# Kernel optimization log

Measured on AMD Instinct MI355X. Metric: run time of the kernel, lower is better.

The kernel has to match this reference:

```python
import jax, jax.numpy as jnp
import numpy as np

HIDDEN = 4096
NUM_BLOCKS = 8
BLOCK = HIDDEN // NUM_BLOCKS  # 512


def setup_inputs() -> dict:
    key = jax.random.key(0)
    k1, k2, k3, k4 = jax.random.split(key, 4)
    return {
        "weight": jax.random.normal(k1, (HIDDEN, HIDDEN), dtype=jnp.float32) * 0.02,
        "bias": jax.random.normal(k2, (HIDDEN,), dtype=jnp.float32) * 0.02,
        "x": jax.random.normal(k3, (4, 2048, HIDDEN), dtype=jnp.float32),
        "proj_R": jax.random.normal(k4, (NUM_BLOCKS, BLOCK, BLOCK), dtype=jnp.float32) * 0.02,
        "layer_idx": 0,
    }


def _cayley_batch(A):
    # Q = (I - S) @ inv(I + S + 1e-6*I), S = 0.5*(A - A^T), batched over blocks
    r = A.shape[-1]
    I = jnp.eye(r, dtype=A.dtype)
    S = 0.5 * (A - jnp.swapaxes(A, -2, -1))
    Minv = jnp.linalg.inv(I + S + 1e-6 * I)
    return jnp.einsum('bij,bjk->bik', I - S, Minv)


def reference(weight, bias, x, proj_R, layer_idx):
    Q = _cayley_batch(proj_R)                     # [nb, bs, bs], orthogonal blocks
    nb, bs, _ = Q.shape
    # block_diag(Q) @ weight == batched block-row matmul (off-diagonal blocks are zero)
    Wb = weight.reshape(nb, bs, weight.shape[1])  # [nb, bs, in]
    filt = jnp.einsum('bij,bjk->bik', Q, Wb).reshape(nb * bs, weight.shape[1])
    # F.linear(x, filt, bias)
    return jnp.einsum('bsi,oi->bso', x, filt) + bias
```

## Files before the change

kernel.cpp:

```cpp
#include <hip/hip_runtime.h>

typedef unsigned short u16;
typedef __attribute__((ext_vector_type(8))) short bf16x8;
typedef __attribute__((ext_vector_type(4))) float f32x4;
typedef __attribute__((ext_vector_type(8))) unsigned short u16x8;
typedef __attribute__((ext_vector_type(4))) unsigned short u16x4;

__device__ __forceinline__ u16 f2bf(float f){
  unsigned int u = __builtin_bit_cast(unsigned int, f);
  u += 0x7FFFu + ((u >> 16) & 1u);
  return (u16)(u >> 16);
}
__device__ __forceinline__ float bf2f(u16 h){
  unsigned int u = ((unsigned int)h) << 16;
  return __builtin_bit_cast(float, u);
}

__device__ __forceinline__ void load16(const u16* g, u16* s){
  __builtin_amdgcn_global_load_lds((const __attribute__((address_space(1))) unsigned int*)g,
                                   (__attribute__((address_space(3))) unsigned int*)s,
                                   16, 0, 0);
}

__global__ __launch_bounds__(256) void build_s(const float* __restrict__ R, u16* __restrict__ Sbf,
                                               u16* __restrict__ Dbf){
  int idx = blockIdx.x * 256 + threadIdx.x;
  int b = idx >> 18;
  int i = (idx >> 9) & 511;
  int j = idx & 511;
  float a  = R[idx];
  float at = R[(b << 18) + (j << 9) + i];
  float s = 0.5f * (a - at);
  Sbf[idx] = f2bf(s);
  Dbf[idx] = f2bf((i == j ? 2.000003f : 0.0f) - 2.000001f * s);
}

__global__ __launch_bounds__(256) void split_p(const float* __restrict__ P, u16* __restrict__ Phl,
                                               u16* __restrict__ X1, u16* __restrict__ X1d){
  int idx = blockIdx.x * 256 + threadIdx.x;
  int i = (idx >> 9) & 511;
  int j = idx & 511;
  float p = P[idx];
  u16 ph = f2bf(p);
  size_t rb = ((size_t)(idx >> 9)) << 10;
  Phl[rb + j]       = ph;
  Phl[rb + 512 + j] = f2bf(p - bf2f(ph));
  const float beta = 0.8264463f;
  u16 x1 = f2bf((i == j ? 2.0f * beta : 0.0f) - beta * beta * p);
  X1[idx] = x1;
  X1d[rb + j]       = x1;
  X1d[rb + 512 + j] = x1;
}

__global__ __launch_bounds__(256) void conv_bf16(const float* __restrict__ src, u16* __restrict__ dst){
  size_t i = (size_t)blockIdx.x * 256 + threadIdx.x;
  const float4* s = (const float4*)src + i * 2;
  float4 v0 = s[0], v1 = s[1];
  u16x8 o = { f2bf(v0.x), f2bf(v0.y), f2bf(v0.z), f2bf(v0.w),
              f2bf(v1.x), f2bf(v1.y), f2bf(v1.z), f2bf(v1.w) };
  *(u16x8*)(dst + i * 8) = o;
}

__global__ __launch_bounds__(256) void transpose_w(const float* __restrict__ W, u16* __restrict__ Wt){
  const int b = blockIdx.z;
  const int i0 = blockIdx.x << 5;
  const int j0 = blockIdx.y << 5;
  __shared__ float tile[32][33];
  const int t = threadIdx.x;
  const int r = t >> 3, c = (t & 7) << 2;
  float4 v = *(const float4*)&W[(size_t)((b << 9) + j0 + r) * 4096 + i0 + c];
  tile[r][c+0] = v.x; tile[r][c+1] = v.y; tile[r][c+2] = v.z; tile[r][c+3] = v.w;
  __syncthreads();
  u16x4 o = { f2bf(tile[c+0][r]), f2bf(tile[c+1][r]), f2bf(tile[c+2][r]), f2bf(tile[c+3][r]) };
  *(u16x4*)&Wt[((size_t)b << 21) + (size_t)(i0 + r) * 512 + j0 + c] = o;
}

template<int EPI>
__global__ __launch_bounds__(256) void gemm_bt(const u16* __restrict__ A, const u16* __restrict__ B,
                                               void* __restrict__ Cout, const void* __restrict__ aux,
                                               int M, int N, int K){
  const int bz = blockIdx.z;
  const u16* Ab = A + (size_t)bz * M * K;
  const u16* Bb = B + (size_t)bz * N * K;
  const int m0 = blockIdx.y << 7, n0 = blockIdx.x << 7;
  __shared__ __align__(16) u16 As[4096];
  __shared__ __align__(16) u16 Bs[4096];
  const int t = threadIdx.x;
  const int w = t >> 6, l = t & 63;
  const int wr = w >> 1, wc = w & 1;
  const int kofs = (l & 3) << 3;
  const int rA = l >> 2;
  const int aRd = ((wr << 6) + (l & 15)) * 32 + ((l >> 4) << 3);
  const int bRd = ((wc << 6) + (l & 15)) * 32 + ((l >> 4) << 3);
  f32x4 acc[4][4] = {};
  for (int k0 = 0; k0 < K; k0 += 32){
#pragma unroll
    for (int j = 0; j < 2; ++j){
      int rowBase = ((w << 1) + j) << 4;
      load16(&Ab[(size_t)(m0 + rowBase + rA) * K + k0 + kofs], &As[((w << 1) + j) << 9]);
      load16(&Bb[(size_t)(n0 + rowBase + rA) * K + k0 + kofs], &Bs[((w << 1) + j) << 9]);
    }
    __syncthreads();
    bf16x8 aF[4], bF[4];
#pragma unroll
    for (int mf = 0; mf < 4; ++mf) aF[mf] = *(const bf16x8*)&As[aRd + (mf << 9)];
#pragma unroll
    for (int nf = 0; nf < 4; ++nf) bF[nf] = *(const bf16x8*)&Bs[bRd + (nf << 9)];
#pragma unroll
    for (int mf = 0; mf < 4; ++mf)
#pragma unroll
      for (int nf = 0; nf < 4; ++nf)
        acc[mf][nf] = __builtin_amdgcn_mfma_f32_16x16x32_bf16(aF[mf], bF[nf], acc[mf][nf], 0, 0, 0);
    __syncthreads();
  }
#pragma unroll
  for (int mf = 0; mf < 4; ++mf){
#pragma unroll
    for (int nf = 0; nf < 4; ++nf){
      const int col = n0 + (wc << 6) + (nf << 4) + (l & 15);
#pragma unroll
      for (int q = 0; q < 4; ++q){
        const int row = m0 + (wr << 6) + (mf << 4) + ((l >> 4) << 2) + q;
        float v = acc[mf][nf][q];
        size_t gi = ((size_t)bz * M + row) * N + col;
        if (EPI == 2){
          ((u16*)Cout)[gi] = f2bf(v);
        } else if (EPI == 3){
          ((u16*)Cout)[gi] = f2bf((row == col ? 2.0f : 0.0f) - v);
        } else if (EPI == 6){
          ((u16*)Cout)[gi] = f2bf(bf2f(((const u16*)aux)[gi]) + v);
        } else if (EPI == 7){
          u16 o = f2bf(v);
          ((u16*)Cout)[gi] = o;
          size_t g2 = (((size_t)bz * M + row) << 10) + col;
          u16* d = (u16*)const_cast<void*>(aux);
          d[g2] = o;
          d[g2 + 512] = o;
        } else if (EPI == 8){
          ((float*)Cout)[gi] = v + (row == col ? 1.000002f : 0.0f);
        } else if (EPI == 9){
          ((u16*)Cout)[gi] = f2bf(v - (row == col ? 1.0f : 0.0f));
        } else {
          ((u16*)Cout)[gi] = f2bf((row == col ? 1.0f : 0.0f) - v);
        }
      }
    }
  }
}

template<int EPI>
__global__ __launch_bounds__(512, 2) void gemm256(const u16* __restrict__ A, const u16* __restrict__ B,
                                                  void* __restrict__ Cout, const float* __restrict__ aux,
                                                  int M, int N, int K){
  __shared__ __align__(16) char lds[131072];
  const int bz = blockIdx.z;
  const char* Ab = (const char*)(A + (size_t)bz * M * K);
  const char* Bb = (const char*)(B + (size_t)bz * N * K);
  const int NB = N >> 8;
  const int nwg = gridDim.x;
  const int bid = blockIdx.x;
  const int swzb = (bid & 7) * (nwg >> 3) + (bid >> 3);
  const int m0 = (swzb / NB) << 8;
  const int n0 = (swzb % NB) << 8;
  const int tid = threadIdx.x;
  const int w = tid >> 6, l = tid & 63;
  const int wm = w >> 2, wn = w & 3;
  const size_t Kb = (size_t)K << 1;
  const int NT = K >> 6;
  const int sRow = tid >> 3;
  const int sCol = ((tid & 7) << 4) ^ ((sRow & 7) << 4);
  const int sDst = tid << 4;
  const char* aS = Ab + (size_t)(m0 + sRow) * Kb + sCol;
  const char* bS = Bb + (size_t)(n0 + sRow) * Kb + sCol;
  const int lrow = (l & 15) << 7;
  const int kq0 = (((l >> 4) << 4)) ^ ((l & 7) << 4);
  const int aOff = (wm << 14) + lrow;
  const int bOff = 32768 + ((wn >> 1) << 14) + ((wn & 1) << 13) + lrow;

#define STAGE_H(isB, h, tt) { \
    const int _lo = (((tt) & 1) << 16) + ((isB) << 15) + ((h) << 14); \
    const char* _s = ((isB) ? bS : aS) + ((size_t)((h) << 7)) * Kb + ((size_t)(tt) << 7); \
    load16((const u16*)_s, (u16*)(lds + _lo + sDst)); \
    load16((const u16*)(_s + (Kb << 6)), (u16*)(lds + _lo + 8192 + sDst)); }

#define RD_A(bufb, UQ) \
  _Pragma("unroll") for (int i2 = 0; i2 < 4; ++i2){ \
    aF[i2][0] = *(const bf16x8*)(lds + (bufb) + aOff + ((UQ) << 13) + (i2 << 11) + kq0); \
    aF[i2][1] = *(const bf16x8*)(lds + (bufb) + aOff + ((UQ) << 13) + (i2 << 11) + (kq0 ^ 64)); }

#define RD_B(bufb, VQ) \
  _Pragma("unroll") for (int j2 = 0; j2 < 2; ++j2){ \
    bF[VQ][j2][0] = *(const bf16x8*)(lds + (bufb) + bOff + ((VQ) << 12) + (j2 << 11) + kq0); \
    bF[VQ][j2][1] = *(const bf16x8*)(lds + (bufb) + bOff + ((VQ) << 12) + (j2 << 11) + (kq0 ^ 64)); }

#define MFMA16(UQ, VQ) \
    _Pragma("unroll") for (int i2 = 0; i2 < 4; ++i2) \
      _Pragma("unroll") for (int j2 = 0; j2 < 2; ++j2){ \
        acc[(UQ)*4+i2][(VQ)*2+j2] = __builtin_amdgcn_mfma_f32_16x16x32_bf16(aF[i2][0], bF[VQ][j2][0], acc[(UQ)*4+i2][(VQ)*2+j2], 0, 0, 0); \
        acc[(UQ)*4+i2][(VQ)*2+j2] = __builtin_amdgcn_mfma_f32_16x16x32_bf16(aF[i2][1], bF[VQ][j2][1], acc[(UQ)*4+i2][(VQ)*2+j2], 0, 0, 0); }

#define BAR asm volatile("s_barrier" ::: "memory");
#define VM4 asm volatile("s_waitcnt vmcnt(4)" ::: "memory");
#define VM0 asm volatile("s_waitcnt vmcnt(0)" ::: "memory");

  bf16x8 aF[4][2], bF[2][2][2];
  f32x4 acc[8][4] = {};

  STAGE_H(0,0,0) STAGE_H(1,0,0) STAGE_H(0,1,0) STAGE_H(1,1,0)
  STAGE_H(0,0,1) STAGE_H(1,0,1)
  VM4 BAR

#define KTILE(t, bufb) { \
    const int t1 = ((t)+1 < NT) ? (t)+1 : NT-1; \
    const int t2 = ((t)+2 < NT) ? (t)+2 : NT-1; \
    RD_A(bufb, 0) RD_B(bufb, 0) STAGE_H(0,1,t1) \
    MFMA16(0,0) \
    RD_B(bufb, 1) STAGE_H(1,1,t1) \
    MFMA16(0,1) \
    RD_A(bufb, 1) STAGE_H(0,0,t2) \
    MFMA16(1,1) \
    STAGE_H(1,0,t2) \
    MFMA16(1,0) \
    __builtin_amdgcn_sched_barrier(0); \
    VM4 BAR }

#pragma unroll 1
  for (int tp = 0; tp < NT; tp += 2){
    KTILE(tp, 0)
    KTILE(tp+1, 65536)
  }
  VM0
#undef KTILE
#undef STAGE_H
#undef RD_A
#undef RD_B
#undef MFMA16
#undef BAR
#undef VM4
#undef VM0

#pragma unroll
  for (int mf = 0; mf < 8; ++mf){
#pragma unroll
    for (int nf = 0; nf < 4; ++nf){
      const int col = n0 + (wn << 6) + (nf << 4) + (l & 15);
#pragma unroll
      for (int q = 0; q < 4; ++q){
        const int row = m0 + (wm << 7) + (mf << 4) + ((l >> 4) << 2) + q;
        float v = acc[mf][nf][q];
        if (EPI == 0){
          ((float*)Cout)[(size_t)row * N + col] = v + aux[col];
        } else {
          ((u16*)Cout)[((size_t)bz * M + row) * N + col] = f2bf(v);
        }
      }
    }
  }
}

extern "C" void kernel_launch(void* const* d_in, const int* in_sizes, int n_in,
                              void* d_out, int out_size, void* d_ws, size_t ws_size,
                              hipStream_t stream){
  const float* W    = (const float*)d_in[0];
  const float* bias = (const float*)d_in[1];
  const float* x    = (const float*)d_in[2];
  const float* R    = (const float*)d_in[3];
  (void)in_sizes; (void)n_in; (void)out_size; (void)ws_size;

  char* ws = (char*)d_ws;
  const size_t MiB = (size_t)1 << 20;
  u16*   Sbf  = (u16*)(ws + 0 * MiB);
  u16*   Dbf  = (u16*)(ws + 4 * MiB);
  float* Pf   = (float*)(ws + 8 * MiB);
  u16*   X1   = (u16*)(ws + 16 * MiB);
  u16*   Ybf  = (u16*)(ws + 20 * MiB);
  u16*   X2   = (u16*)(ws + 24 * MiB);
  u16*   Phl  = (u16*)(ws + 28 * MiB);
  u16*   X2d  = (u16*)(ws + 36 * MiB);
  u16*   X1d  = (u16*)(ws + 44 * MiB);
  u16*   Rbf  = X1;
  u16*   X3   = Ybf;
  u16*   G    = Sbf;
  u16*   Wt   = (u16*)(ws + 8 * MiB);
  u16*   filt = (u16*)(ws + 64 * MiB);
  u16*   xbf  = (u16*)(ws + 0 * MiB);

  const dim3 gNS(4, 4, 8);

  build_s<<<8192, 256, 0, stream>>>(R, Sbf, Dbf);
  gemm_bt<8><<<gNS, 256, 0, stream>>>(Sbf, Sbf, Pf, nullptr, 512, 512, 512);
  split_p<<<8192, 256, 0, stream>>>(Pf, Phl, X1, X1d);
  gemm_bt<3><<<gNS, 256, 0, stream>>>(Phl, X1d, Ybf, nullptr, 512, 512, 1024);
  gemm_bt<7><<<gNS, 256, 0, stream>>>(X1, Ybf, X2, X2d, 512, 512, 512);
  gemm_bt<10><<<gNS, 256, 0, stream>>>(Phl, X2d, Rbf, nullptr, 512, 512, 1024);
  gemm_bt<6><<<gNS, 256, 0, stream>>>(X2, Rbf, X3, X2, 512, 512, 512);
  gemm_bt<9><<<gNS, 256, 0, stream>>>(Dbf, X3, G, nullptr, 512, 512, 512);
  transpose_w<<<dim3(128, 16, 8), 256, 0, stream>>>(W, Wt);
  gemm256<2><<<dim3(32, 1, 8), 512, 0, stream>>>(G, Wt, (void*)filt, nullptr, 512, 4096, 512);
  conv_bf16<<<16384, 256, 0, stream>>>(x, xbf);
  gemm256<0><<<dim3(512, 1, 1), 512, 0, stream>>>(xbf, filt, d_out, bias, 8192, 4096, 4096);
}
```

Baseline: 412.0 us.

## Fuse split_p into S·Sᵀ GEMM epilogue and simplify gemm256 prefetch pipeline

Removes the separate split_p kernel by computing the hi/lo bf16 split and the X1 initial-guess terms directly in the epilogue of the first small GEMM. This drops an fp32 intermediate round trip and a launch. Separately, the big gemm256 main loop changes from a two-tile-ahead prefetch with vmcnt(4) waits to a one-tile-ahead prefetch with full vmcnt(0) waits each tile. The shallower pipeline exposes more global-load latency in the dominant 8192x4096x4096 GEMM.

```diff
diff --git a/kernel.cpp b/kernel.cpp
--- a/kernel.cpp
+++ b/kernel.cpp
@@ -33,23 +33,6 @@
   float s = 0.5f * (a - at);
   Sbf[idx] = f2bf(s);
   Dbf[idx] = f2bf((i == j ? 2.000003f : 0.0f) - 2.000001f * s);
-}
-
-__global__ __launch_bounds__(256) void split_p(const float* __restrict__ P, u16* __restrict__ Phl,
-                                               u16* __restrict__ X1, u16* __restrict__ X1d){
-  int idx = blockIdx.x * 256 + threadIdx.x;
-  int i = (idx >> 9) & 511;
-  int j = idx & 511;
-  float p = P[idx];
-  u16 ph = f2bf(p);
-  size_t rb = ((size_t)(idx >> 9)) << 10;
-  Phl[rb + j]       = ph;
-  Phl[rb + 512 + j] = f2bf(p - bf2f(ph));
-  const float beta = 0.8264463f;
-  u16 x1 = f2bf((i == j ? 2.0f * beta : 0.0f) - beta * beta * p);
-  X1[idx] = x1;
-  X1d[rb + j]       = x1;
-  X1d[rb + 512 + j] = x1;
 }
 
 __global__ __launch_bounds__(256) void conv_bf16(const float* __restrict__ src, u16* __restrict__ dst){
@@ -78,6 +61,7 @@
 template<int EPI>
 __global__ __launch_bounds__(256) void gemm_bt(const u16* __restrict__ A, const u16* __restrict__ B,
                                                void* __restrict__ Cout, const void* __restrict__ aux,
+                                               void* __restrict__ aux2,
                                                int M, int N, int K){
   const int bz = blockIdx.z;
   const u16* Ab = A + (size_t)bz * M * K;
@@ -123,25 +107,31 @@
         const int row = m0 + (wr << 6) + (mf << 4) + ((l >> 4) << 2) + q;
         float v = acc[mf][nf][q];
         size_t gi = ((size_t)bz * M + row) * N + col;
-        if (EPI == 2){
-          ((u16*)Cout)[gi] = f2bf(v);
-        } else if (EPI == 3){
+        size_t g2 = (((size_t)bz * M + row) << 10) + col;
+        if (EPI == 3){
           ((u16*)Cout)[gi] = f2bf((row == col ? 2.0f : 0.0f) - v);
         } else if (EPI == 6){
           ((u16*)Cout)[gi] = f2bf(bf2f(((const u16*)aux)[gi]) + v);
         } else if (EPI == 7){
           u16 o = f2bf(v);
           ((u16*)Cout)[gi] = o;
-          size_t g2 = (((size_t)bz * M + row) << 10) + col;
           u16* d = (u16*)const_cast<void*>(aux);
           d[g2] = o;
           d[g2 + 512] = o;
-        } else if (EPI == 8){
-          ((float*)Cout)[gi] = v + (row == col ? 1.000002f : 0.0f);
         } else if (EPI == 9){
           ((u16*)Cout)[gi] = f2bf(v - (row == col ? 1.0f : 0.0f));
+        } else if (EPI == 10){
+          ((u16*)Cout)[gi] = f2bf((row == col ? 1.0f : 0.0f) - v);
         } else {
-          ((u16*)Cout)[gi] = f2bf((row == col ? 1.0f : 0.0f) - v);
+          float p = v + (row == col ? 1.000002f : 0.0f);
+          u16 ph = f2bf(p);
+          ((u16*)Cout)[g2] = ph;
+          ((u16*)Cout)[g2 + 512] = f2bf(p - bf2f(ph));
+          const float beta = 0.8264463f;
+          u16 x1 = f2bf((row == col ? 2.0f * beta : 0.0f) - beta * beta * p);
+          ((u16*)const_cast<void*>(aux))[gi] = x1;
+          ((u16*)aux2)[g2] = x1;
+          ((u16*)aux2)[g2 + 512] = x1;
         }
       }
     }
@@ -200,43 +190,38 @@
         acc[(UQ)*4+i2][(VQ)*2+j2] = __builtin_amdgcn_mfma_f32_16x16x32_bf16(aF[i2][1], bF[VQ][j2][1], acc[(UQ)*4+i2][(VQ)*2+j2], 0, 0, 0); }
 
 #define BAR asm volatile("s_barrier" ::: "memory");
-#define VM4 asm volatile("s_waitcnt vmcnt(4)" ::: "memory");
 #define VM0 asm volatile("s_waitcnt vmcnt(0)" ::: "memory");
 
   bf16x8 aF[4][2], bF[2][2][2];
   f32x4 acc[8][4] = {};
 
   STAGE_H(0,0,0) STAGE_H(1,0,0) STAGE_H(0,1,0) STAGE_H(1,1,0)
-  STAGE_H(0,0,1) STAGE_H(1,0,1)
-  VM4 BAR
+  VM0 BAR
 
 #define KTILE(t, bufb) { \
-    const int t1 = ((t)+1 < NT) ? (t)+1 : NT-1; \
-    const int t2 = ((t)+2 < NT) ? (t)+2 : NT-1; \
-    RD_A(bufb, 0) RD_B(bufb, 0) STAGE_H(0,1,t1) \
+    RD_A(bufb, 0) RD_B(bufb, 0) \
+    if ((t) + 1 < NT) { STAGE_H(0,0,(t)+1) STAGE_H(1,0,(t)+1) } \
     MFMA16(0,0) \
-    RD_B(bufb, 1) STAGE_H(1,1,t1) \
+    RD_B(bufb, 1) \
+    if ((t) + 1 < NT) { STAGE_H(0,1,(t)+1) STAGE_H(1,1,(t)+1) } \
     MFMA16(0,1) \
-    RD_A(bufb, 1) STAGE_H(0,0,t2) \
+    RD_A(bufb, 1) \
     MFMA16(1,1) \
-    STAGE_H(1,0,t2) \
     MFMA16(1,0) \
     __builtin_amdgcn_sched_barrier(0); \
-    VM4 BAR }
+    VM0 BAR }
 
 #pragma unroll 1
   for (int tp = 0; tp < NT; tp += 2){
     KTILE(tp, 0)
     KTILE(tp+1, 65536)
   }
-  VM0
 #undef KTILE
 #undef STAGE_H
 #undef RD_A
 #undef RD_B
 #undef MFMA16
 #undef BAR
-#undef VM4
 #undef VM0
 
 #pragma unroll
@@ -271,7 +256,6 @@
   const size_t MiB = (size_t)1 << 20;
   u16*   Sbf  = (u16*)(ws + 0 * MiB);
   u16*   Dbf  = (u16*)(ws + 4 * MiB);
-  float* Pf   = (float*)(ws + 8 * MiB);
   u16*   X1   = (u16*)(ws + 16 * MiB);
   u16*   Ybf  = (u16*)(ws + 20 * MiB);
   u16*   X2   = (u16*)(ws + 24 * MiB);
@@ -288,13 +272,12 @@
   const dim3 gNS(4, 4, 8);
 
   build_s<<<8192, 256, 0, stream>>>(R, Sbf, Dbf);
-  gemm_bt<8><<<gNS, 256, 0, stream>>>(Sbf, Sbf, Pf, nullptr, 512, 512, 512);
-  split_p<<<8192, 256, 0, stream>>>(Pf, Phl, X1, X1d);
-  gemm_bt<3><<<gNS, 256, 0, stream>>>(Phl, X1d, Ybf, nullptr, 512, 512, 1024);
-  gemm_bt<7><<<gNS, 256, 0, stream>>>(X1, Ybf, X2, X2d, 512, 512, 512);
-  gemm_bt<10><<<gNS, 256, 0, stream>>>(Phl, X2d, Rbf, nullptr, 512, 512, 1024);
-  gemm_bt<6><<<gNS, 256, 0, stream>>>(X2, Rbf, X3, X2, 512, 512, 512);
-  gemm_bt<9><<<gNS, 256, 0, stream>>>(Dbf, X3, G, nullptr, 512, 512, 512);
+  gemm_bt<11><<<gNS, 256, 0, stream>>>(Sbf, Sbf, Phl, X1, X1d, 512, 512, 512);
+  gemm_bt<3><<<gNS, 256, 0, stream>>>(Phl, X1d, Ybf, nullptr, nullptr, 512, 512, 1024);
+  gemm_bt<7><<<gNS, 256, 0, stream>>>(X1, Ybf, X2, X2d, nullptr, 512, 512, 512);
+  gemm_bt<10><<<gNS, 256, 0, stream>>>(Phl, X2d, Rbf, nullptr, nullptr, 512, 512, 1024);
+  gemm_bt<6><<<gNS, 256, 0, stream>>>(X2, Rbf, X3, X2, nullptr, 512, 512, 512);
+  gemm_bt<9><<<gNS, 256, 0, stream>>>(Dbf, X3, G, nullptr, nullptr, 512, 512, 512);
   transpose_w<<<dim3(128, 16, 8), 256, 0, stream>>>(W, Wt);
   gemm256<2><<<dim3(32, 1, 8), 512, 0, stream>>>(G, Wt, (void*)filt, nullptr, 512, 4096, 512);
   conv_bf16<<<16384, 256, 0, stream>>>(x, xbf);
```

New measurement: 410.5 us. No clear change (-0.4%).
